# Optimization experiments

Hardware: AMD Instinct MI355X
Metric: run time of the kernel (lower is better)

Reference implementation:

```python
import jax, jax.numpy as jnp
import numpy as np
from jax import lax

PAD = 1
T, B, V, E, H, K = 256, 64, 50000, 300, 256, 20  # H = hidden_dim//2 per direction


def setup_inputs() -> dict:
    key = jax.random.key(0)
    ks = jax.random.split(key, 14)
    lengths = jnp.sort(jax.random.randint(ks[0], (B,), T // 2, T + 1))[::-1]  # sorted desc like pack_padded
    toks = jax.random.randint(ks[1], (T, B), 2, V)
    tpos = jnp.arange(T)[:, None]
    x = jnp.where(tpos < lengths[None, :], toks, PAD)
    n = jax.random.normal
    s = 1.0 / np.sqrt(H)
    emb = (n(ks[2], (V, E)) * 0.1).at[PAD].set(0.0)  # padding_idx row zeroed
    Wih0 = n(ks[3], (2, 4 * H, E)) * s       # [dir, 4H, in]
    Whh0 = n(ks[4], (2, 4 * H, H)) * s
    b0 = n(ks[5], (2, 4 * H)) * s            # b_ih + b_hh folded together
    Wih1 = n(ks[6], (2, 4 * H, 2 * H)) * s
    Whh1 = n(ks[7], (2, 4 * H, H)) * s
    b1 = n(ks[8], (2, 4 * H)) * s
    W_out = n(ks[9], (K, 2 * H)) * s
    b_out = n(ks[10], (K,)) * s
    trans = n(ks[11], (K, K)) * 0.1
    start = n(ks[12], (K,)) * 0.1
    end = n(ks[13], (K,)) * 0.1
    return dict(x=x, sent_lengths=lengths, emb=emb, Wih0=Wih0, Whh0=Whh0, b0=b0,
                Wih1=Wih1, Whh1=Whh1, b1=b1, W_out=W_out, b_out=b_out,
                trans=trans, start=start, end=end)


def _lstm_dir(xs, m, Wih, Whh, b):
    # xs [T,B,D], m [T,B,1] float mask. PyTorch gate order i,f,g,o.
    xg = jnp.einsum('tbd,gd->tbg', xs, Wih) + b  # big GEMM up-front
    h0 = jnp.zeros((xs.shape[1], H), xs.dtype)

    def step(carry, inp):
        h, c = carry
        g_t, m_t = inp
        gates = g_t + h @ Whh.T
        i, f, g, o = jnp.split(gates, 4, -1)
        c_new = jax.nn.sigmoid(f) * c + jax.nn.sigmoid(i) * jnp.tanh(g)
        h_new = jax.nn.sigmoid(o) * jnp.tanh(c_new)
        # freeze state at padded steps (pack_padded semantics); padded outputs are zero
        return (jnp.where(m_t > 0, h_new, h), jnp.where(m_t > 0, c_new, c)), h_new * m_t

    _, out = lax.scan(step, (h0, h0), (xg, m))
    return out


def _bilstm(xs, m, rev, Wih, Whh, b):
    out_f = _lstm_dir(xs, m, Wih[0], Whh[0], b[0])
    xs_r = jnp.take_along_axis(xs, rev[:, :, None], 0)  # reverse within each length
    out_b = jnp.take_along_axis(_lstm_dir(xs_r, m, Wih[1], Whh[1], b[1]), rev[:, :, None], 0)
    return jnp.concatenate([out_f, out_b], -1)


def reference(x, sent_lengths, emb, Wih0, Whh0, b0, Wih1, Whh1, b1, W_out, b_out, trans, start, end):
    mask = x != PAD                               # [T,B]
    m = mask[:, :, None].astype(emb.dtype)
    tpos = jnp.arange(T)[:, None]
    rev = jnp.where(tpos < sent_lengths[None, :], sent_lengths[None, :] - 1 - tpos, tpos)
    h = emb[x]                                    # [T,B,E]
    h = _bilstm(h, m, rev, Wih0, Whh0, b0)
    h = _bilstm(h, m, rev, Wih1, Whh1, b1)
    emis = jnp.einsum('tbh,kh->tbk', h, W_out) + b_out  # [T,B,K]

    # Viterbi decode (torchcrf semantics)
    score0 = start[None, :] + emis[0]             # [B,K]

    def vstep(sc, inp):
        e_t, m_t = inp
        cand = sc[:, :, None] + trans[None] + e_t[:, None, :]  # [B,prev,next]
        best = cand.max(1)
        ptr = cand.argmax(1).astype(jnp.int32)
        sc2 = jnp.where(m_t[:, None], best, sc)
        # identity pointer at padded steps so backtrace passes tags through
        ptr = jnp.where(m_t[:, None], ptr, jnp.arange(K, dtype=jnp.int32)[None, :])
        return sc2, ptr

    score, hist = lax.scan(vstep, score0, (emis[1:], mask[1:]))
    score = score + end[None, :]                  # score frozen at seq end -> same as adding at last valid step
    last = jnp.argmax(score, -1).astype(jnp.int32)

    def back(tag, ptr):
        prev = jnp.take_along_axis(ptr, tag[:, None], 1)[:, 0]
        return prev, prev

    _, tags_prev = lax.scan(back, last, hist, reverse=True)
    tags = jnp.concatenate([tags_prev, last[None, :]], 0)  # [T,B]
    return jnp.where(mask, tags, 0)
```

## Files before the change

kernel.cpp:

```cpp
#include <hip/hip_runtime.h>
#include <stdint.h>


#define T_ 256
#define B_ 64
#define EPAD 304
#define KTAG 20
#define TB_ (T_ * B_)

#define KR 64
#define KL 12
#define KLQ 3
#define NQS 45
#define WLDS_OFF (2 * KR * 1024)
#define WSTR_OFF (WLDS_OFF + 2 * KLQ * 1024 * 4)

__device__ __forceinline__ float rlane(float v, int l) {
  return __int_as_float(__builtin_amdgcn_readlane(__float_as_int(v), l));
}


__global__ void prep_embed(const int* __restrict__ x, const float* __restrict__ emb,
                           float* __restrict__ xsA) {
  int r = blockIdx.x;
  int tok = x[r];
  const float* src = emb + (size_t)tok * 300;
  for (int e = threadIdx.x; e < EPAD; e += 64)
    xsA[(size_t)r * EPAD + e] = (e < 300) ? src[e] : 0.f;
}

__global__ void prep_b0t(const float* __restrict__ Wih0, float* __restrict__ B0t) {
  int idx = blockIdx.x * 256 + threadIdx.x;
  if (idx >= 2048 * EPAD) return;
  int n = idx / EPAD, k = idx % EPAD;
  B0t[idx] = (k < 300) ? Wih0[(size_t)n * 300 + k] : 0.f;
}

__global__ void prep_bot64(const float* __restrict__ Wout, float* __restrict__ Bot,
                           const float* __restrict__ bout, float* __restrict__ biaso) {
  int idx = blockIdx.x * 256 + threadIdx.x;
  int n = idx >> 9, k = idx & 511;
  Bot[idx] = (n < KTAG) ? Wout[(size_t)n * 512 + k] : 0.f;
  if (idx < 64) biaso[idx] = (idx < KTAG) ? bout[idx] : 0.f;
}

__global__ void prep_whh2(const float* __restrict__ Whh, float* __restrict__ whhL) {
  int idx = blockIdx.x * 256 + threadIdx.x;
  int d = idx >> 18, rem = idx & 262143, k = rem >> 10, tg = rem & 1023;
  int row = (tg & 3) * 256 + (tg >> 2);
  float v = Whh[(size_t)d * 262144 + (size_t)row * 256 + k];
  if (k < KR) {
    whhL[(size_t)(d * KR + k) * 1024 + tg] = v;
  } else if (k < KR + KL) {
    int kk = k - KR, q = kk >> 2, e = kk & 3;
    whhL[WLDS_OFF + (size_t)((d * KLQ + q) * 1024 + tg) * 4 + e] = v;
  } else {
    int kk = k - KR - KL, q = kk >> 2, e = kk & 3;
    whhL[WSTR_OFF + (size_t)((d * NQS + q) * 1024 + tg) * 4 + e] = v;
  }
}

__global__ __launch_bounds__(256) void gemm_f32(
    const float* __restrict__ A, int lda, const float* __restrict__ Bt, int ldb,
    float* __restrict__ C, int ldc, const float* __restrict__ bias,
    int ntn, int K) {
  const int tm = blockIdx.x / ntn, tn = blockIdx.x % ntn;
  const int m0 = tm * 64, n0 = tn * 64;
  __shared__ __align__(16) float As[16][64];
  __shared__ __align__(16) float Bs[16][64];
  const int tid = threadIdx.x;
  const int mm = tid >> 2, kq = (tid & 3) * 4;
  const int tx = tid & 15, ty = tid >> 4;
  float acc[4][4] = {};
  for (int k0 = 0; k0 < K; k0 += 16) {
    float4 av = *(const float4*)&A[(size_t)(m0 + mm) * lda + k0 + kq];
    float4 bv = *(const float4*)&Bt[(size_t)(n0 + mm) * ldb + k0 + kq];
    __syncthreads();
    As[kq + 0][mm] = av.x; As[kq + 1][mm] = av.y;
    As[kq + 2][mm] = av.z; As[kq + 3][mm] = av.w;
    Bs[kq + 0][mm] = bv.x; Bs[kq + 1][mm] = bv.y;
    Bs[kq + 2][mm] = bv.z; Bs[kq + 3][mm] = bv.w;
    __syncthreads();
#pragma unroll
    for (int kk = 0; kk < 16; ++kk) {
      float4 a4 = *(const float4*)&As[kk][ty * 4];
      float4 b4 = *(const float4*)&Bs[kk][tx * 4];
      acc[0][0] += a4.x * b4.x; acc[0][1] += a4.x * b4.y;
      acc[0][2] += a4.x * b4.z; acc[0][3] += a4.x * b4.w;
      acc[1][0] += a4.y * b4.x; acc[1][1] += a4.y * b4.y;
      acc[1][2] += a4.y * b4.z; acc[1][3] += a4.y * b4.w;
      acc[2][0] += a4.z * b4.x; acc[2][1] += a4.z * b4.y;
      acc[2][2] += a4.z * b4.z; acc[2][3] += a4.z * b4.w;
      acc[3][0] += a4.w * b4.x; acc[3][1] += a4.w * b4.y;
      acc[3][2] += a4.w * b4.z; acc[3][3] += a4.w * b4.w;
    }
  }
#pragma unroll
  for (int i = 0; i < 4; ++i)
#pragma unroll
    for (int j = 0; j < 4; ++j)
      C[(size_t)(m0 + ty * 4 + i) * ldc + n0 + tx * 4 + j] =
          acc[i][j] + bias[n0 + tx * 4 + j];
}

__global__ __launch_bounds__(1024, 4) void lstm_rec(
    const float* __restrict__ xg, const float* __restrict__ whhL,
    float* __restrict__ out, const int* __restrict__ lens) {
  const int wg = blockIdx.x, dir = wg & 1, b = wg >> 1;
  const int len = lens[b];
  const int tg = threadIdx.x;
  const int j = tg >> 2, gt = tg & 3;
  const int row = gt * 256 + j;

  float wres[KR];
#pragma unroll
  for (int k = 0; k < KR; ++k)
    wres[k] = whhL[(size_t)(dir * KR + k) * 1024 + tg];

  __shared__ __align__(16) float4 wlds[KLQ][1024];
  __shared__ __align__(16) float hsd[2][256];
#pragma unroll
  for (int q = 0; q < KLQ; ++q)
    wlds[q][tg] = *(const float4*)&whhL[WLDS_OFF + (size_t)((dir * KLQ + q) * 1024 + tg) * 4];
  if (tg < 256) hsd[0][tg] = 0.f;
  float c = 0.f;
  __syncthreads();

  const float* sp = whhL + WSTR_OFF + (size_t)dir * NQS * 4096 + (size_t)tg * 4;

  const int lane = tg & 63, qb = lane & ~3;

  for (int s = 0; s < len; ++s) {
    const int t = dir ? (len - 1 - s) : s;
    const int rp = t * B_ + b;
    float xv = xg[(size_t)rp * 2048 + dir * 1024 + row];
    float4 hv = *(const float4*)&hsd[s & 1][lane * 4];

    float acc0 = 0.f, acc1 = 0.f;
#pragma unroll
    for (int q = 0; q < KR / 4; ++q) {
      float b0 = rlane(hv.x, q), b1 = rlane(hv.y, q);
      float b2 = rlane(hv.z, q), b3 = rlane(hv.w, q);
      acc0 += wres[4 * q + 0] * b0 + wres[4 * q + 1] * b1;
      acc1 += wres[4 * q + 2] * b2 + wres[4 * q + 3] * b3;
    }
#pragma unroll
    for (int q3 = 0; q3 < KLQ; ++q3) {
      int q = KR / 4 + q3;
      float4 wl = wlds[q3][tg];
      float b0 = rlane(hv.x, q), b1 = rlane(hv.y, q);
      float b2 = rlane(hv.z, q), b3 = rlane(hv.w, q);
      acc0 += wl.x * b0 + wl.y * b1;
      acc1 += wl.z * b2 + wl.w * b3;
    }
#pragma unroll 5
    for (int qq = 0; qq < NQS; ++qq) {
      int q = KR / 4 + KLQ + qq;
      float4 wv = *(const float4*)(sp + (size_t)qq * 4096);
      float b0 = rlane(hv.x, q), b1 = rlane(hv.y, q);
      float b2 = rlane(hv.z, q), b3 = rlane(hv.w, q);
      acc0 += wv.x * b0 + wv.y * b1;
      acc1 += wv.z * b2 + wv.w * b3;
    }

    float a = acc0 + acc1 + xv;
    float v1 = __shfl(a, qb | 1);
    float v2 = __shfl(a, qb | 2);
    float v3 = __shfl(a, qb | 3);
    if (gt == 0) {
      float si = 1.f / (1.f + expf(-a));
      float sf = 1.f / (1.f + expf(-v1));
      float so = 1.f / (1.f + expf(-v3));
      c = sf * c + si * tanhf(v2);
      float h = so * tanhf(c);
      hsd[(s + 1) & 1][j] = h;
      out[(size_t)rp * 512 + dir * 256 + j] = h;
    }
    __syncthreads();
  }
  for (int t = len; t < T_; ++t)
    if (gt == 0) out[(size_t)(t * B_ + b) * 512 + dir * 256 + j] = 0.f;
}

__global__ __launch_bounds__(64) void viterbi(
    const float* __restrict__ emis, const float* __restrict__ trans,
    const float* __restrict__ startv, const float* __restrict__ endv,
    const int* __restrict__ lens, int* __restrict__ outp) {
  int b = blockIdx.x, lane = threadIdx.x;
  __shared__ float tr[KTAG * KTAG];
  __shared__ float fin[KTAG];
  __shared__ unsigned char hist[T_ * KTAG];
  for (int i = lane; i < KTAG * KTAG; i += 64) tr[i] = trans[i];
  int len = lens[b];
  float score = (lane < KTAG) ? startv[lane] + emis[(size_t)b * 64 + lane] : -3e38f;
  __syncthreads();
  for (int t = 1; t < len; ++t) {
    float e = (lane < KTAG) ? emis[(size_t)(t * B_ + b) * 64 + lane] : 0.f;
    float best = -3e38f; int bp = 0;
    for (int p = 0; p < KTAG; ++p) {
      float cand = (__shfl(score, p) + tr[p * KTAG + lane]) + e;
      if (cand > best) { best = cand; bp = p; }
    }
    if (lane < KTAG) { score = best; hist[t * KTAG + lane] = (unsigned char)bp; }
  }
  if (lane < KTAG) fin[lane] = score + endv[lane];
  __syncthreads();
  if (lane == 0) {
    float bb = -3e38f; int tag = 0;
    for (int p = 0; p < KTAG; ++p)
      if (fin[p] > bb) { bb = fin[p]; tag = p; }
    for (int t = len - 1; t >= 1; --t) {
      outp[t * B_ + b] = tag;
      tag = hist[t * KTAG + tag];
    }
    outp[b] = tag;
  }
  for (int t = len + lane; t < T_; t += 64) outp[t * B_ + b] = 0;
}

__global__ void sentinel_fill(int* __restrict__ outp, int val) {
  int i = blockIdx.x * 256 + threadIdx.x;
  if (i < TB_) outp[i] = val;
}
__global__ void diag_init(int* __restrict__ f) { if (threadIdx.x == 0) f[0] = 0; }
__global__ void check_nan(const float* __restrict__ p, long n, int* __restrict__ f) {
  long i0 = (long)blockIdx.x * 256 + threadIdx.x;
  int bad = 0;
  for (long i = i0; i < n; i += (long)gridDim.x * 256)
    if (!(fabsf(p[i]) <= 1e8f)) bad = 1;
  if (bad) atomicOr(&f[0], 1);
}
__global__ void verdict(const int* __restrict__ f, int* __restrict__ outp) {
  if (f[0]) outp[threadIdx.x] = -4096;
}


extern "C" void kernel_launch(void* const* d_in, const int* in_sizes, int n_in,
                              void* d_out, int out_size, void* d_ws, size_t ws_size,
                              hipStream_t stream) {
  int* outp = (int*)d_out;

  static const int exp_sizes[14] = {16384, 64, 15000000, 614400, 524288, 2048,
                                    1048576, 524288, 2048, 10240, 20, 400, 20, 20};
  int badi = (n_in == 14) ? -1 : 14;
  if (badi < 0)
    for (int i = 0; i < 14; ++i)
      if (in_sizes[i] != exp_sizes[i]) { badi = i; break; }
  if (badi >= 0) {
    hipLaunchKernelGGL(sentinel_fill, dim3((TB_ + 255) / 256), dim3(256), 0, stream,
                       outp, -(20000 + badi));
    return;
  }

  const int*   x      = (const int*)d_in[0];
  const int*   lens   = (const int*)d_in[1];
  const float* emb    = (const float*)d_in[2];
  const float* Wih0   = (const float*)d_in[3];
  const float* Whh0   = (const float*)d_in[4];
  const float* b0     = (const float*)d_in[5];
  const float* Wih1   = (const float*)d_in[6];
  const float* Whh1   = (const float*)d_in[7];
  const float* b1     = (const float*)d_in[8];
  const float* Wout   = (const float*)d_in[9];
  const float* bout   = (const float*)d_in[10];
  const float* trans  = (const float*)d_in[11];
  const float* startv = (const float*)d_in[12];
  const float* endv   = (const float*)d_in[13];

  const size_t sz_whh = (size_t)524288 * 4;

  const size_t need =
      (size_t)TB_ * 2048 * 4
    + (size_t)TB_ * EPAD * 4
    + (size_t)TB_ * 512 * 4
    + (size_t)2048 * EPAD * 4
    + (size_t)64 * 512 * 4
    + 2 * sz_whh
    + 64 * 4
    + (size_t)TB_ * 64 * 4
    + 64;

  if (ws_size < need) {
    hipLaunchKernelGGL(sentinel_fill, dim3((TB_ + 255) / 256), dim3(256), 0, stream,
                       outp, -(int)(10000 + (ws_size >> 20)));
    return;
  }

  char* w = (char*)d_ws;
  float* xg    = (float*)w;  w += (size_t)TB_ * 2048 * 4;
  float* xsA   = (float*)w;  w += (size_t)TB_ * EPAD * 4;
  float* outh  = (float*)w;  w += (size_t)TB_ * 512 * 4;
  float* B0t   = (float*)w;  w += (size_t)2048 * EPAD * 4;
  float* Bot   = (float*)w;  w += (size_t)64 * 512 * 4;
  float* whh0L = (float*)w;  w += sz_whh;
  float* whh1L = (float*)w;  w += sz_whh;
  float* biaso = (float*)w;  w += 64 * 4;
  float* emis  = (float*)w;  w += (size_t)TB_ * 64 * 4;
  int*   diag  = (int*)w;    w += 64;

  hipLaunchKernelGGL(diag_init, dim3(1), dim3(64), 0, stream, diag);
  hipLaunchKernelGGL(prep_embed, dim3(TB_), dim3(64), 0, stream, x, emb, xsA);
  hipLaunchKernelGGL(prep_b0t, dim3((2048 * EPAD + 255) / 256), dim3(256), 0, stream, Wih0, B0t);
  hipLaunchKernelGGL(prep_bot64, dim3(128), dim3(256), 0, stream, Wout, Bot, bout, biaso);
  hipLaunchKernelGGL(prep_whh2, dim3(2048), dim3(256), 0, stream, Whh0, whh0L);
  hipLaunchKernelGGL(prep_whh2, dim3(2048), dim3(256), 0, stream, Whh1, whh1L);

  hipLaunchKernelGGL(gemm_f32, dim3(256 * 32), dim3(256), 0, stream,
                     xsA, EPAD, B0t, EPAD, xg, 2048, b0, 32, EPAD);
  hipLaunchKernelGGL(lstm_rec, dim3(128), dim3(1024), 0, stream, xg, whh0L, outh, lens);
  hipLaunchKernelGGL(gemm_f32, dim3(256 * 32), dim3(256), 0, stream,
                     outh, 512, Wih1, 512, xg, 2048, b1, 32, 512);
  hipLaunchKernelGGL(lstm_rec, dim3(128), dim3(1024), 0, stream, xg, whh1L, outh, lens);
  hipLaunchKernelGGL(gemm_f32, dim3(256), dim3(256), 0, stream,
                     outh, 512, Bot, 512, emis, 64, biaso, 1, 512);
  hipLaunchKernelGGL(check_nan, dim3(256), dim3(256), 0, stream,
                     emis, (long)TB_ * 64, diag);
  hipLaunchKernelGGL(viterbi, dim3(B_), dim3(64), 0, stream,
                     emis, trans, startv, endv, lens, outp);
  hipLaunchKernelGGL(verdict, dim3(1), dim3(64), 0, stream, diag, outp);
}
```

Measured before the change: 4.778 ms.

## Add 256-thread LSTM recurrence kernel keeping more Whh in registers, with runtime fallback

Adds a new recurrence kernel where each thread owns one hidden unit and computes all four gates, so the per-step cross-lane shuffles are gone. It holds 25 of the 64 weight quads per gate in registers (up to 512 VGPRs at one wave per EU), 9 in LDS, and streams the rest from global memory, using a new weight layout. A host-side check of the compiled register count and spill size picks this kernel or the old 1024-thread one. The trade is less parallelism per block and more global weight streaming per thread, in exchange for more register-resident weights and simpler gate handling.

```diff
diff --git a/kernel.cpp b/kernel.cpp
--- a/kernel.cpp
+++ b/kernel.cpp
@@ -8,12 +8,15 @@
 #define KTAG 20
 #define TB_ (T_ * B_)
 
-#define KR 64
-#define KL 12
-#define KLQ 3
-#define NQS 45
-#define WLDS_OFF (2 * KR * 1024)
-#define WSTR_OFF (WLDS_OFF + 2 * KLQ * 1024 * 4)
+#define QRH 25
+#define QLH 9
+#define QSH 30
+
+#define KR_LO 64
+#define KLQ_LO 3
+#define NQS_LO 45
+#define WLDS_OFF_LO (2 * KR_LO * 1024)
+#define WSTR_OFF_LO (WLDS_OFF_LO + 2 * KLQ_LO * 1024 * 4)
 
 __device__ __forceinline__ float rlane(float v, int l) {
   return __int_as_float(__builtin_amdgcn_readlane(__float_as_int(v), l));
@@ -44,19 +47,28 @@
   if (idx < 64) biaso[idx] = (idx < KTAG) ? bout[idx] : 0.f;
 }
 
+__global__ void prep_whh4(const float* __restrict__ Whh, float* __restrict__ whhU) {
+  int idx = blockIdx.x * 256 + threadIdx.x;
+  int d = idx >> 18, rem = idx & 262143, row = rem >> 8, k = rem & 255;
+  float v = Whh[(size_t)d * 262144 + (size_t)row * 256 + k];
+  int gt = row >> 8, j = row & 255;
+  int q = k >> 2, e = k & 3;
+  whhU[((((size_t)d * 64 + q) * 4 + gt) * 256 + j) * 4 + e] = v;
+}
+
 __global__ void prep_whh2(const float* __restrict__ Whh, float* __restrict__ whhL) {
   int idx = blockIdx.x * 256 + threadIdx.x;
   int d = idx >> 18, rem = idx & 262143, k = rem >> 10, tg = rem & 1023;
   int row = (tg & 3) * 256 + (tg >> 2);
   float v = Whh[(size_t)d * 262144 + (size_t)row * 256 + k];
-  if (k < KR) {
-    whhL[(size_t)(d * KR + k) * 1024 + tg] = v;
-  } else if (k < KR + KL) {
-    int kk = k - KR, q = kk >> 2, e = kk & 3;
-    whhL[WLDS_OFF + (size_t)((d * KLQ + q) * 1024 + tg) * 4 + e] = v;
+  if (k < KR_LO) {
+    whhL[(size_t)(d * KR_LO + k) * 1024 + tg] = v;
+  } else if (k < KR_LO + 12) {
+    int kk = k - KR_LO, q = kk >> 2, e = kk & 3;
+    whhL[WLDS_OFF_LO + (size_t)((d * KLQ_LO + q) * 1024 + tg) * 4 + e] = v;
   } else {
-    int kk = k - KR - KL, q = kk >> 2, e = kk & 3;
-    whhL[WSTR_OFF + (size_t)((d * NQS + q) * 1024 + tg) * 4 + e] = v;
+    int kk = k - KR_LO - 12, q = kk >> 2, e = kk & 3;
+    whhL[WSTR_OFF_LO + (size_t)((d * NQS_LO + q) * 1024 + tg) * 4 + e] = v;
   }
 }
 
@@ -103,7 +115,108 @@
           acc[i][j] + bias[n0 + tx * 4 + j];
 }
 
-__global__ __launch_bounds__(1024, 4) void lstm_rec(
+__global__ __attribute__((amdgpu_flat_work_group_size(256, 256),
+                          amdgpu_waves_per_eu(1, 1)))
+void lstm_rec_hi(const float* __restrict__ xg, const float* __restrict__ whhU,
+                 float* __restrict__ out, const int* __restrict__ lens) {
+  const int wg = blockIdx.x, d = wg & 1, b = wg >> 1;
+  const int len = lens[b];
+  const int j = threadIdx.x;
+  const int l = j & 63;
+  const float* wb = whhU + (size_t)d * 64 * 4096;
+
+  float4 wr[QRH][4];
+#pragma unroll
+  for (int q = 0; q < QRH; ++q)
+#pragma unroll
+    for (int g = 0; g < 4; ++g)
+      wr[q][g] = *(const float4*)(wb + ((size_t)(q * 4 + g) * 256 + j) * 4);
+#pragma unroll
+  for (int q = 0; q < QRH; ++q)
+#pragma unroll
+    for (int g = 0; g < 4; ++g)
+      asm volatile("" : "+v"(wr[q][g].x), "+v"(wr[q][g].y),
+                        "+v"(wr[q][g].z), "+v"(wr[q][g].w));
+
+  __shared__ __align__(16) float4 wlds[QLH][4][256];
+  __shared__ __align__(16) float hsd[2][256];
+  for (int i = j; i < QLH * 4 * 256; i += 256) {
+    int q3 = i >> 10, g = (i >> 8) & 3, jj = i & 255;
+    wlds[q3][g][jj] =
+        *(const float4*)(wb + ((size_t)((QRH + q3) * 4 + g) * 256 + jj) * 4);
+  }
+  hsd[0][j] = 0.f;
+  float c = 0.f;
+  __syncthreads();
+
+  const float* sp = wb + (size_t)j * 4;
+
+  for (int s = 0; s < len; ++s) {
+    const int t = d ? (len - 1 - s) : s;
+    const int rp = t * B_ + b;
+    const size_t xb = (size_t)rp * 2048 + d * 1024 + j;
+    float xv0 = xg[xb];
+    float xv1 = xg[xb + 256];
+    float xv2 = xg[xb + 512];
+    float xv3 = xg[xb + 768];
+    float4 hv = *(const float4*)&hsd[s & 1][l * 4];
+
+    float ai0 = 0.f, ai1 = 0.f, af0 = 0.f, af1 = 0.f;
+    float ag0 = 0.f, ag1 = 0.f, ao0 = 0.f, ao1 = 0.f;
+#pragma unroll
+    for (int q = 0; q < QRH; ++q) {
+      float b0 = rlane(hv.x, q), b1 = rlane(hv.y, q);
+      float b2 = rlane(hv.z, q), b3 = rlane(hv.w, q);
+      ai0 += wr[q][0].x * b0 + wr[q][0].y * b1; ai1 += wr[q][0].z * b2 + wr[q][0].w * b3;
+      af0 += wr[q][1].x * b0 + wr[q][1].y * b1; af1 += wr[q][1].z * b2 + wr[q][1].w * b3;
+      ag0 += wr[q][2].x * b0 + wr[q][2].y * b1; ag1 += wr[q][2].z * b2 + wr[q][2].w * b3;
+      ao0 += wr[q][3].x * b0 + wr[q][3].y * b1; ao1 += wr[q][3].z * b2 + wr[q][3].w * b3;
+    }
+#pragma unroll
+    for (int q3 = 0; q3 < QLH; ++q3) {
+      int q = QRH + q3;
+      float b0 = rlane(hv.x, q), b1 = rlane(hv.y, q);
+      float b2 = rlane(hv.z, q), b3 = rlane(hv.w, q);
+      float4 wi = wlds[q3][0][j], wf = wlds[q3][1][j];
+      float4 wg2 = wlds[q3][2][j], wo = wlds[q3][3][j];
+      ai0 += wi.x * b0 + wi.y * b1;  ai1 += wi.z * b2 + wi.w * b3;
+      af0 += wf.x * b0 + wf.y * b1;  af1 += wf.z * b2 + wf.w * b3;
+      ag0 += wg2.x * b0 + wg2.y * b1; ag1 += wg2.z * b2 + wg2.w * b3;
+      ao0 += wo.x * b0 + wo.y * b1;  ao1 += wo.z * b2 + wo.w * b3;
+    }
+#pragma unroll 5
+    for (int qs = 0; qs < QSH; ++qs) {
+      int q = QRH + QLH + qs;
+      float b0 = rlane(hv.x, q), b1 = rlane(hv.y, q);
+      float b2 = rlane(hv.z, q), b3 = rlane(hv.w, q);
+      float4 wi = *(const float4*)(sp + (size_t)(q * 4 + 0) * 1024);
+      float4 wf = *(const float4*)(sp + (size_t)(q * 4 + 1) * 1024);
+      float4 wg2 = *(const float4*)(sp + (size_t)(q * 4 + 2) * 1024);
+      float4 wo = *(const float4*)(sp + (size_t)(q * 4 + 3) * 1024);
+      ai0 += wi.x * b0 + wi.y * b1;  ai1 += wi.z * b2 + wi.w * b3;
+      af0 += wf.x * b0 + wf.y * b1;  af1 += wf.z * b2 + wf.w * b3;
+      ag0 += wg2.x * b0 + wg2.y * b1; ag1 += wg2.z * b2 + wg2.w * b3;
+      ao0 += wo.x * b0 + wo.y * b1;  ao1 += wo.z * b2 + wo.w * b3;
+    }
+
+    float a0 = ai0 + ai1 + xv0;
+    float a1 = af0 + af1 + xv1;
+    float a2 = ag0 + ag1 + xv2;
+    float a3 = ao0 + ao1 + xv3;
+    float si = 1.f / (1.f + expf(-a0));
+    float sf = 1.f / (1.f + expf(-a1));
+    float so = 1.f / (1.f + expf(-a3));
+    c = sf * c + si * tanhf(a2);
+    float h = so * tanhf(c);
+    hsd[(s + 1) & 1][j] = h;
+    out[(size_t)rp * 512 + d * 256 + j] = h;
+    __syncthreads();
+  }
+  for (int t = len; t < T_; ++t)
+    out[(size_t)(t * B_ + b) * 512 + d * 256 + j] = 0.f;
+}
+
+__global__ __launch_bounds__(1024, 4) void lstm_rec_lo(
     const float* __restrict__ xg, const float* __restrict__ whhL,
     float* __restrict__ out, const int* __restrict__ lens) {
   const int wg = blockIdx.x, dir = wg & 1, b = wg >> 1;
@@ -112,22 +225,21 @@
   const int j = tg >> 2, gt = tg & 3;
   const int row = gt * 256 + j;
 
-  float wres[KR];
-#pragma unroll
-  for (int k = 0; k < KR; ++k)
-    wres[k] = whhL[(size_t)(dir * KR + k) * 1024 + tg];
-
-  __shared__ __align__(16) float4 wlds[KLQ][1024];
+  float wres[KR_LO];
+#pragma unroll
+  for (int k = 0; k < KR_LO; ++k)
+    wres[k] = whhL[(size_t)(dir * KR_LO + k) * 1024 + tg];
+
+  __shared__ __align__(16) float4 wlds[KLQ_LO][1024];
   __shared__ __align__(16) float hsd[2][256];
 #pragma unroll
-  for (int q = 0; q < KLQ; ++q)
-    wlds[q][tg] = *(const float4*)&whhL[WLDS_OFF + (size_t)((dir * KLQ + q) * 1024 + tg) * 4];
+  for (int q = 0; q < KLQ_LO; ++q)
+    wlds[q][tg] = *(const float4*)&whhL[WLDS_OFF_LO + (size_t)((dir * KLQ_LO + q) * 1024 + tg) * 4];
   if (tg < 256) hsd[0][tg] = 0.f;
   float c = 0.f;
   __syncthreads();
 
-  const float* sp = whhL + WSTR_OFF + (size_t)dir * NQS * 4096 + (size_t)tg * 4;
-
+  const float* sp = whhL + WSTR_OFF_LO + (size_t)dir * NQS_LO * 4096 + (size_t)tg * 4;
   const int lane = tg & 63, qb = lane & ~3;
 
   for (int s = 0; s < len; ++s) {
@@ -138,15 +250,15 @@
 
     float acc0 = 0.f, acc1 = 0.f;
 #pragma unroll
-    for (int q = 0; q < KR / 4; ++q) {
+    for (int q = 0; q < KR_LO / 4; ++q) {
       float b0 = rlane(hv.x, q), b1 = rlane(hv.y, q);
       float b2 = rlane(hv.z, q), b3 = rlane(hv.w, q);
       acc0 += wres[4 * q + 0] * b0 + wres[4 * q + 1] * b1;
       acc1 += wres[4 * q + 2] * b2 + wres[4 * q + 3] * b3;
     }
 #pragma unroll
-    for (int q3 = 0; q3 < KLQ; ++q3) {
-      int q = KR / 4 + q3;
+    for (int q3 = 0; q3 < KLQ_LO; ++q3) {
+      int q = KR_LO / 4 + q3;
       float4 wl = wlds[q3][tg];
       float b0 = rlane(hv.x, q), b1 = rlane(hv.y, q);
       float b2 = rlane(hv.z, q), b3 = rlane(hv.w, q);
@@ -154,8 +266,8 @@
       acc1 += wl.z * b2 + wl.w * b3;
     }
 #pragma unroll 5
-    for (int qq = 0; qq < NQS; ++qq) {
-      int q = KR / 4 + KLQ + qq;
+    for (int qq = 0; qq < NQS_LO; ++qq) {
+      int q = KR_LO / 4 + KLQ_LO + qq;
       float4 wv = *(const float4*)(sp + (size_t)qq * 4096);
       float b0 = rlane(hv.x, q), b1 = rlane(hv.y, q);
       float b2 = rlane(hv.z, q), b3 = rlane(hv.w, q);
@@ -267,6 +379,16 @@
   const float* startv = (const float*)d_in[12];
   const float* endv   = (const float*)d_in[13];
 
+  static int chosen = -1;
+  if (chosen < 0) {
+    chosen = 0;
+    hipFuncAttributes fa;
+    if (hipFuncGetAttributes(&fa, reinterpret_cast<const void*>(&lstm_rec_hi)) ==
+            hipSuccess &&
+        fa.localSizeBytes == 0 && fa.numRegs >= 430)
+      chosen = 1;
+  }
+
   const size_t sz_whh = (size_t)524288 * 4;
 
   const size_t need =
@@ -275,7 +397,7 @@
     + (size_t)TB_ * 512 * 4
     + (size_t)2048 * EPAD * 4
     + (size_t)64 * 512 * 4
-    + 2 * sz_whh
+    + 4 * sz_whh
     + 64 * 4
     + (size_t)TB_ * 64 * 4
     + 64;
@@ -292,6 +414,8 @@
   float* outh  = (float*)w;  w += (size_t)TB_ * 512 * 4;
   float* B0t   = (float*)w;  w += (size_t)2048 * EPAD * 4;
   float* Bot   = (float*)w;  w += (size_t)64 * 512 * 4;
+  float* whh0U = (float*)w;  w += sz_whh;
+  float* whh1U = (float*)w;  w += sz_whh;
   float* whh0L = (float*)w;  w += sz_whh;
   float* whh1L = (float*)w;  w += sz_whh;
   float* biaso = (float*)w;  w += 64 * 4;
@@ -302,15 +426,26 @@
   hipLaunchKernelGGL(prep_embed, dim3(TB_), dim3(64), 0, stream, x, emb, xsA);
   hipLaunchKernelGGL(prep_b0t, dim3((2048 * EPAD + 255) / 256), dim3(256), 0, stream, Wih0, B0t);
   hipLaunchKernelGGL(prep_bot64, dim3(128), dim3(256), 0, stream, Wout, Bot, bout, biaso);
-  hipLaunchKernelGGL(prep_whh2, dim3(2048), dim3(256), 0, stream, Whh0, whh0L);
-  hipLaunchKernelGGL(prep_whh2, dim3(2048), dim3(256), 0, stream, Whh1, whh1L);
+  if (chosen == 1) {
+    hipLaunchKernelGGL(prep_whh4, dim3(2048), dim3(256), 0, stream, Whh0, whh0U);
+    hipLaunchKernelGGL(prep_whh4, dim3(2048), dim3(256), 0, stream, Whh1, whh1U);
+  } else {
+    hipLaunchKernelGGL(prep_whh2, dim3(2048), dim3(256), 0, stream, Whh0, whh0L);
+    hipLaunchKernelGGL(prep_whh2, dim3(2048), dim3(256), 0, stream, Whh1, whh1L);
+  }
 
   hipLaunchKernelGGL(gemm_f32, dim3(256 * 32), dim3(256), 0, stream,
                      xsA, EPAD, B0t, EPAD, xg, 2048, b0, 32, EPAD);
-  hipLaunchKernelGGL(lstm_rec, dim3(128), dim3(1024), 0, stream, xg, whh0L, outh, lens);
+  if (chosen == 1)
+    hipLaunchKernelGGL(lstm_rec_hi, dim3(128), dim3(256), 0, stream, xg, whh0U, outh, lens);
+  else
+    hipLaunchKernelGGL(lstm_rec_lo, dim3(128), dim3(1024), 0, stream, xg, whh0L, outh, lens);
   hipLaunchKernelGGL(gemm_f32, dim3(256 * 32), dim3(256), 0, stream,
                      outh, 512, Wih1, 512, xg, 2048, b1, 32, 512);
-  hipLaunchKernelGGL(lstm_rec, dim3(128), dim3(1024), 0, stream, xg, whh1L, outh, lens);
+  if (chosen == 1)
+    hipLaunchKernelGGL(lstm_rec_hi, dim3(128), dim3(256), 0, stream, xg, whh1U, outh, lens);
+  else
+    hipLaunchKernelGGL(lstm_rec_lo, dim3(128), dim3(1024), 0, stream, xg, whh1L, outh, lens);
   hipLaunchKernelGGL(gemm_f32, dim3(256), dim3(256), 0, stream,
                      outh, 512, Bot, 512, emis, 64, biaso, 1, 512);
   hipLaunchKernelGGL(check_nan, dim3(256), dim3(256), 0, stream,
```

Measured after the change: 5.255 ms. 1.1x slower.
